# Kernel optimization log

Measured on AMD Instinct MI355X. Metric: run time of the kernel, lower is better.

The kernel has to match this reference:

```python
import jax, jax.numpy as jnp
import numpy as np

N = 20000
E = 320000
IN_DIM, HID, MID, OUT, HEADS = 1536, 512, 128, 5, 8
NEG_SLOPE = 0.2
BN_EPS = 1e-5


def gat_conv(x, edge_index, W, a_src, a_dst, bias, heads, out_ch):
    """PyG-style GATConv (eval mode, self-loops already in edge_index).
    x: [N, F_in]; W: [F_in, heads*out_ch]; a_src/a_dst: [heads, out_ch]; bias: [heads*out_ch].
    Returns [N, heads*out_ch] (head concat)."""
    n = x.shape[0]
    h = (x @ W).reshape(n, heads, out_ch)              # [N,H,C]
    src, dst = edge_index[0], edge_index[1]
    al_s = jnp.sum(h * a_src, axis=-1)                 # [N,H]
    al_d = jnp.sum(h * a_dst, axis=-1)                 # [N,H]
    e = al_s[src] + al_d[dst]                          # [E,H]
    e = jnp.where(e >= 0, e, NEG_SLOPE * e)            # leaky_relu
    # segment softmax over incoming edges per dst node
    e_max = jax.ops.segment_max(e, dst, num_segments=n)
    e_max = jnp.where(jnp.isfinite(e_max), e_max, 0.0)
    ex = jnp.exp(e - e_max[dst])                       # [E,H]
    denom = jax.ops.segment_sum(ex, dst, num_segments=n)
    alpha = ex / (denom[dst] + 1e-16)                  # [E,H]
    msg = h[src] * alpha[:, :, None]                   # [E,H,C]
    out = jax.ops.segment_sum(msg, dst, num_segments=n)
    return out.reshape(n, heads * out_ch) + bias


def bn_eval(x, gamma, beta, mean, var):
    return (x - mean) * jax.lax.rsqrt(var + BN_EPS) * gamma + beta


def setup_inputs() -> dict:
    key = jax.random.key(0)
    ks = jax.random.split(key, 24)
    x = jax.random.normal(ks[0], (N, IN_DIM), dtype=jnp.float32)
    edge_index = jax.random.randint(ks[1], (2, E), 0, N, dtype=jnp.int32)

    def glorot(k, shape):
        fan = shape[0] + shape[-1]
        return jax.random.normal(k, shape, dtype=jnp.float32) * np.sqrt(2.0 / fan)

    inp = {"x": x, "edge_index": edge_index}
    # conv1: 1536 -> 8 heads x 64
    inp["W1"] = glorot(ks[2], (IN_DIM, HID))
    inp["as1"] = glorot(ks[3], (HEADS, HID // HEADS))
    inp["ad1"] = glorot(ks[4], (HEADS, HID // HEADS))
    inp["b1"] = jnp.zeros((HID,), jnp.float32)
    # conv2: 512 -> 8 heads x 16
    inp["W2"] = glorot(ks[5], (HID, MID))
    inp["as2"] = glorot(ks[6], (HEADS, MID // HEADS))
    inp["ad2"] = glorot(ks[7], (HEADS, MID // HEADS))
    inp["b2"] = jnp.zeros((MID,), jnp.float32)
    # conv3: 128 -> 1 head x 5
    inp["W3"] = glorot(ks[8], (MID, OUT))
    inp["as3"] = glorot(ks[9], (1, OUT))
    inp["ad3"] = glorot(ks[10], (1, OUT))
    inp["b3"] = jnp.zeros((OUT,), jnp.float32)
    # batchnorm params (eval mode, running stats)
    inp["g1"] = jax.random.normal(ks[11], (HID,), jnp.float32) * 0.1 + 1.0
    inp["be1"] = jax.random.normal(ks[12], (HID,), jnp.float32) * 0.1
    inp["m1"] = jax.random.normal(ks[13], (HID,), jnp.float32) * 0.1
    inp["v1"] = jax.random.uniform(ks[14], (HID,), jnp.float32, 0.5, 1.5)
    inp["g2"] = jax.random.normal(ks[15], (MID,), jnp.float32) * 0.1 + 1.0
    inp["be2"] = jax.random.normal(ks[16], (MID,), jnp.float32) * 0.1
    inp["m2"] = jax.random.normal(ks[17], (MID,), jnp.float32) * 0.1
    inp["v2"] = jax.random.uniform(ks[18], (MID,), jnp.float32, 0.5, 1.5)
    return inp


def reference(x, edge_index, W1, as1, ad1, b1, W2, as2, ad2, b2, W3, as3, ad3, b3,
              g1, be1, m1, v1, g2, be2, m2, v2):
    # add self-loops (PyG GATConv default)
    loops = jnp.arange(N, dtype=edge_index.dtype)
    ei = jnp.concatenate([edge_index, jnp.stack([loops, loops])], axis=1)

    h = jax.nn.relu(gat_conv(x, ei, W1, as1, ad1, b1, HEADS, HID // HEADS))
    h = bn_eval(h, g1, be1, m1, v1)
    h = jax.nn.relu(gat_conv(h, ei, W2, as2, ad2, b2, HEADS, MID // HEADS))
    h = bn_eval(h, g2, be2, m2, v2)
    h = gat_conv(h, ei, W3, as3, ad3, b3, 1, OUT)
    return jax.nn.log_softmax(h, axis=1)
```

## Files before the change

### kernel.cpp

```cpp
#include <hip/hip_runtime.h>
#include <math.h>

#define IN_DIM 1536
#define HID 512
#define MID 128
#define OUTC 5
#define HEADS 8
#define NEG_SLOPE 0.2f
#define BN_EPS 1e-5f

typedef __attribute__((ext_vector_type(8))) short s16x8;
typedef __attribute__((ext_vector_type(4))) float fx4;

__device__ __forceinline__ unsigned short bf16_rne(float f) {
    unsigned int u = __float_as_uint(f);
    u += 0x7fffu + ((u >> 16) & 1u);
    return (unsigned short)(u >> 16);
}
__device__ __forceinline__ float bf16_to_f32(unsigned short u) {
    return __uint_as_float((unsigned int)u << 16);
}

__device__ __forceinline__ void async_copy16(void* lds, const void* g) {
    __builtin_amdgcn_global_load_lds(
        (const __attribute__((address_space(1))) unsigned int*)g,
        (__attribute__((address_space(3))) unsigned int*)lds, 16, 0, 0);
}

__global__ void hist_kernel(const int* __restrict__ ei, int* __restrict__ deg,
                            int ET, int E) {
    int e = blockIdx.x * blockDim.x + threadIdx.x;
    if (e >= ET) return;
    int dst = (e < E) ? ei[E + e] : (e - E);
    atomicAdd(&deg[dst], 1);
}

__global__ __launch_bounds__(1024) void scan_kernel(const int* __restrict__ deg,
                                                    int* __restrict__ row_ptr,
                                                    int* __restrict__ cursor, int n) {
    __shared__ int sdata[20000];
    __shared__ int partial[1024];
    int tid = threadIdx.x;
    for (int i = tid; i < n; i += 1024) sdata[i] = deg[i];
    __syncthreads();
    int per = (n + 1023) / 1024;
    int base = tid * per;
    int s = 0;
    for (int i = 0; i < per; ++i) {
        int idx = base + i;
        if (idx < n) s += sdata[idx];
    }
    partial[tid] = s;
    __syncthreads();
    for (int off = 1; off < 1024; off <<= 1) {
        int v = (tid >= off) ? partial[tid - off] : 0;
        __syncthreads();
        partial[tid] += v;
        __syncthreads();
    }
    int prefix = (tid == 0) ? 0 : partial[tid - 1];
    for (int i = 0; i < per; ++i) {
        int idx = base + i;
        if (idx < n) {
            int d = sdata[idx];
            sdata[idx] = prefix;
            prefix += d;
        }
    }
    __syncthreads();
    for (int i = tid; i < n; i += 1024) {
        int v = sdata[i];
        row_ptr[i] = v;
        cursor[i] = v;
    }
    if (tid == 1023) row_ptr[n] = partial[1023];
}

__global__ void scatter_kernel(const int* __restrict__ ei, int* __restrict__ cursor,
                               int* __restrict__ csr_src, int ET, int E) {
    int e = blockIdx.x * blockDim.x + threadIdx.x;
    if (e >= ET) return;
    int src, dst;
    if (e < E) { src = ei[e]; dst = ei[E + e]; }
    else       { src = dst = e - E; }
    int slot = atomicAdd(&cursor[dst], 1);
    csr_src[slot] = src;
}

#define ZB 20
__global__ __launch_bounds__(256) void prep_kernel(
    int* __restrict__ deg, int n_deg4,
    const float* __restrict__ W1, unsigned short* __restrict__ W1h,
    const float* __restrict__ W2, unsigned short* __restrict__ W2h,
    unsigned short* __restrict__ W2l,
    const float* __restrict__ x, unsigned short* __restrict__ xh, int n4) {
    int b = blockIdx.x;
    if (b < ZB) {
        int i = b * 256 + threadIdx.x;
        if (i < n_deg4) ((int4*)deg)[i] = make_int4(0, 0, 0, 0);
        return;
    }
    if (b < ZB + 832) {
        __shared__ float tile[32][33];
        int tb = b - ZB;
        const float* W;
        unsigned short *Th, *Tl;
        int K, Nn, kb, nb;
        bool wlo;
        if (tb < 768) {
            W = W1; Th = W1h; Tl = nullptr; wlo = false; K = IN_DIM; Nn = HID;
            nb = (tb & 15) * 32; kb = (tb >> 4) * 32;
        } else {
            int b2 = tb - 768;
            W = W2; Th = W2h; Tl = W2l; wlo = true; K = HID; Nn = MID;
            nb = (b2 & 3) * 32; kb = (b2 >> 2) * 32;
        }
        int tx = threadIdx.x & 31, ty = threadIdx.x >> 5;
#pragma unroll
        for (int r = 0; r < 4; ++r)
            tile[ty + r * 8][tx] = W[(size_t)(kb + ty + r * 8) * Nn + nb + tx];
        __syncthreads();
#pragma unroll
        for (int r = 0; r < 4; ++r) {
            int n = ty + r * 8;
            float v = tile[tx][n];
            unsigned short hi = bf16_rne(v);
            size_t o = (size_t)(nb + n) * K + kb + tx;
            Th[o] = hi;
            if (wlo) {
                float hif = __uint_as_float((unsigned int)hi << 16);
                Tl[o] = bf16_rne(v - hif);
            }
        }
        return;
    }
    int i = (b - ZB - 832) * 256 + threadIdx.x;
    if (i >= n4) return;
    float4 v = ((const float4*)x)[i];
    ushort4 o;
    o.x = bf16_rne(v.x); o.y = bf16_rne(v.y);
    o.z = bf16_rne(v.z); o.w = bf16_rne(v.w);
    ((ushort4*)xh)[i] = o;
}

__global__ __launch_bounds__(256) void gemm1_kernel(
    const unsigned short* __restrict__ A, const unsigned short* __restrict__ Bh,
    unsigned short* __restrict__ Cb, const float* __restrict__ a_s,
    const float* __restrict__ a_d, float* __restrict__ als,
    float* __restrict__ ald, int M, int N, int K, int MBLK) {
    int b = blockIdx.x;
    int xm = (b & 7) + 8 * (b >> 4);
    int ym = (b >> 3) & 1;
    if (xm >= MBLK) return;

    __shared__ unsigned short Asb[2][64 * 32];
    __shared__ unsigned short Bsb[2][256 * 32];

    const int tid = threadIdx.x;
    const int lane = tid & 63;
    const int wv = tid >> 6;
    const int row0 = xm * 64;
    const int nb0 = ym * 256;
    const int col = lane & 15;
    const int quad = lane >> 4;
    const int n0 = wv * 64;

    const int s_row = lane >> 2;
    const int s_chunk = (lane & 3) ^ ((lane >> 3) & 3);
    int agr = row0 + wv * 16 + s_row; if (agr >= M) agr = M - 1;
    const size_t ag = (size_t)agr * K + s_chunk * 8;
    size_t bg[4];
#pragma unroll
    for (int t = 0; t < 4; ++t)
        bg[t] = (size_t)(nb0 + (wv * 4 + t) * 16 + s_row) * K + s_chunk * 8;

    const int rsw = (col >> 1) & 3;

    fx4 acc[4][4];
#pragma unroll
    for (int i = 0; i < 4; ++i)
#pragma unroll
        for (int j = 0; j < 4; ++j) acc[i][j] = (fx4){0.f, 0.f, 0.f, 0.f};

    async_copy16(&Asb[0][wv * 512], A + ag);
#pragma unroll
    for (int t = 0; t < 4; ++t)
        async_copy16(&Bsb[0][(wv * 4 + t) * 512], Bh + bg[t]);
    __syncthreads();

    int cur = 0;
    for (int k0 = 0; k0 < K; k0 += 32) {
        const int nxt = cur ^ 1;
        if (k0 + 32 < K) {
            const int kn = k0 + 32;
            async_copy16(&Asb[nxt][wv * 512], A + ag + kn);
#pragma unroll
            for (int t = 0; t < 4; ++t)
                async_copy16(&Bsb[nxt][(wv * 4 + t) * 512], Bh + bg[t] + kn);
        }
        s16x8 afr[4], bfr[4];
#pragma unroll
        for (int i = 0; i < 4; ++i)
            afr[i] = *(const s16x8*)&Asb[cur][(i * 16 + col) * 32 + (quad ^ rsw) * 8];
#pragma unroll
        for (int j = 0; j < 4; ++j)
            bfr[j] = *(const s16x8*)&Bsb[cur][(n0 + j * 16 + col) * 32 + (quad ^ rsw) * 8];
#pragma unroll
        for (int i = 0; i < 4; ++i)
#pragma unroll
            for (int j = 0; j < 4; ++j)
                acc[i][j] = __builtin_amdgcn_mfma_f32_16x16x32_bf16(afr[i], bfr[j], acc[i][j], 0, 0, 0);
        __syncthreads();
        cur = nxt;
    }

#pragma unroll
    for (int i = 0; i < 4; ++i) {
        int gr0 = row0 + i * 16 + quad * 4;
#pragma unroll
        for (int j = 0; j < 4; ++j) {
            int gc = nb0 + n0 + j * 16 + col;
#pragma unroll
            for (int r = 0; r < 4; ++r) {
                int gr = gr0 + r;
                if (gr < M) Cb[(size_t)gr * N + gc] = bf16_rne(acc[i][j][r]);
            }
        }
    }

    const int head = (nb0 + n0) >> 6;
    float asv[4], adv[4];
#pragma unroll
    for (int j = 0; j < 4; ++j) {
        asv[j] = a_s[head * 64 + j * 16 + col];
        adv[j] = a_d[head * 64 + j * 16 + col];
    }
#pragma unroll
    for (int i = 0; i < 4; ++i) {
#pragma unroll
        for (int r = 0; r < 4; ++r) {
            float ss = acc[i][0][r] * asv[0] + acc[i][1][r] * asv[1] +
                       acc[i][2][r] * asv[2] + acc[i][3][r] * asv[3];
            float sd = acc[i][0][r] * adv[0] + acc[i][1][r] * adv[1] +
                       acc[i][2][r] * adv[2] + acc[i][3][r] * adv[3];
#pragma unroll
            for (int off = 8; off; off >>= 1) {
                ss += __shfl_xor(ss, off);
                sd += __shfl_xor(sd, off);
            }
            if (col == 0) {
                int gr = row0 + i * 16 + quad * 4 + r;
                if (gr < M) {
                    als[gr * HEADS + head] = ss;
                    ald[gr * HEADS + head] = sd;
                }
            }
        }
    }
}

__global__ __launch_bounds__(256) void gemm2_kernel(
    const unsigned short* __restrict__ A, const unsigned short* __restrict__ Bh,
    const unsigned short* __restrict__ Bl, unsigned short* __restrict__ Cb,
    const float* __restrict__ a_s, const float* __restrict__ a_d,
    float* __restrict__ als, float* __restrict__ ald, int M, int N, int K) {
    __shared__ unsigned short Asb[2][32 * 32];
    __shared__ unsigned short Bhb[2][128 * 32];
    __shared__ unsigned short Blb[2][128 * 32];

    const int tid = threadIdx.x;
    const int lane = tid & 63;
    const int wv = tid >> 6;
    const int row0 = blockIdx.x * 32;
    const int col = lane & 15;
    const int quad = lane >> 4;
    const int m0 = (wv >> 1) * 16;
    const int n0 = (wv & 1) * 64;
    const int b_row = lane >> 2;
    const int b_chunk = (lane & 3) ^ ((lane >> 3) & 3);
    const int rsw = (col >> 1) & 3;

    const int t0 = wv * 2, t1 = t0 + 1;
    const size_t bgo0 = (size_t)(t0 * 16 + b_row) * K + b_chunk * 8;
    const size_t bgo1 = (size_t)(t1 * 16 + b_row) * K + b_chunk * 8;
    int agr = row0 + wv * 16 + b_row; if (agr >= M) agr = M - 1;
    const size_t ago = (size_t)agr * K + b_chunk * 8;

    fx4 acc[4];
#pragma unroll
    for (int j = 0; j < 4; ++j) acc[j] = (fx4){0.f, 0.f, 0.f, 0.f};

    auto stage = [&](int buf, int k) {
        async_copy16(&Bhb[buf][t0 * 512], Bh + bgo0 + k);
        async_copy16(&Bhb[buf][t1 * 512], Bh + bgo1 + k);
        async_copy16(&Blb[buf][t0 * 512], Bl + bgo0 + k);
        async_copy16(&Blb[buf][t1 * 512], Bl + bgo1 + k);
        if (wv < 2) async_copy16(&Asb[buf][wv * 512], A + ago + k);
    };

    stage(0, 0);
    __syncthreads();

    int cur = 0;
    for (int k0 = 0; k0 < K; k0 += 32) {
        const int nxt = cur ^ 1;
        if (k0 + 32 < K) stage(nxt, k0 + 32);
        s16x8 a, bh4[4], bl4[4];
        a = *(const s16x8*)&Asb[cur][(m0 + col) * 32 + (quad ^ rsw) * 8];
#pragma unroll
        for (int j = 0; j < 4; ++j) {
            int rb = (n0 + j * 16 + col) * 32 + (quad ^ rsw) * 8;
            bh4[j] = *(const s16x8*)&Bhb[cur][rb];
            bl4[j] = *(const s16x8*)&Blb[cur][rb];
        }
#pragma unroll
        for (int j = 0; j < 4; ++j) {
            acc[j] = __builtin_amdgcn_mfma_f32_16x16x32_bf16(a, bl4[j], acc[j], 0, 0, 0);
            acc[j] = __builtin_amdgcn_mfma_f32_16x16x32_bf16(a, bh4[j], acc[j], 0, 0, 0);
        }
        __syncthreads();
        cur = nxt;
    }

    int gr0 = row0 + m0 + quad * 4;
#pragma unroll
    for (int j = 0; j < 4; ++j) {
        int gc = n0 + j * 16 + col;
#pragma unroll
        for (int r = 0; r < 4; ++r) {
            int gr = gr0 + r;
            if (gr < M) Cb[(size_t)gr * N + gc] = bf16_rne(acc[j][r]);
        }
    }

    float asv[4], adv[4];
#pragma unroll
    for (int j = 0; j < 4; ++j) {
        asv[j] = a_s[n0 + j * 16 + col];
        adv[j] = a_d[n0 + j * 16 + col];
    }
#pragma unroll
    for (int j = 0; j < 4; ++j) {
        int head = (n0 >> 4) + j;
#pragma unroll
        for (int r = 0; r < 4; ++r) {
            float ss = acc[j][r] * asv[j];
            float sd = acc[j][r] * adv[j];
#pragma unroll
            for (int off = 8; off; off >>= 1) {
                ss += __shfl_xor(ss, off);
                sd += __shfl_xor(sd, off);
            }
            if (col == 0) {
                int gr = gr0 + r;
                if (gr < M) {
                    als[gr * HEADS + head] = ss;
                    ald[gr * HEADS + head] = sd;
                }
            }
        }
    }
}

__global__ __launch_bounds__(256) void agg1_wave_kernel(
    const unsigned short* __restrict__ hlin, const float* __restrict__ als,
    const float* __restrict__ ald, const int* __restrict__ row_ptr,
    const int* __restrict__ csr_src, const float* __restrict__ bias,
    const float* __restrict__ gamma, const float* __restrict__ beta,
    const float* __restrict__ mean, const float* __restrict__ var,
    unsigned short* __restrict__ outh, int n) {
    int lane = threadIdx.x & 63;
    int dst = blockIdx.x * 4 + (threadIdx.x >> 6);
    if (dst >= n) return;
    const int f0 = lane * 8;
    const int h = lane >> 3;
    const int j8 = lane >> 3;
    const int ch = lane & 7;
    float ald_c = ald[dst * HEADS + ch];

    int s0 = row_ptr[dst], s1 = row_ptr[dst + 1];
    float acc[8];
#pragma unroll
    for (int v = 0; v < 8; ++v) acc[v] = 0.f;
    float den = 0.f;

    for (int base = s0; base < s1; base += 8) {
        int take = min(8, s1 - base);
        float ex = 0.f;
        int src_l = 0;
        if (j8 < take) {
            src_l = csr_src[base + j8];
            float e = als[src_l * HEADS + ch] + ald_c;
            e = (e >= 0.f) ? e : NEG_SLOPE * e;
            ex = __expf(e);
        }
        s16x8 rows[8];
#pragma unroll
        for (int jj = 0; jj < 8; ++jj) {
            if (jj < take) {
                int src = __shfl(src_l, jj * 8);
                rows[jj] = *(const s16x8*)&hlin[(size_t)src * HID + f0];
            }
        }
#pragma unroll
        for (int jj = 0; jj < 8; ++jj) {
            if (jj < take) {
                float a = __shfl(ex, jj * 8 + h);
                den += a;
                union { s16x8 v; unsigned short u[8]; } w;
                w.v = rows[jj];
#pragma unroll
                for (int v = 0; v < 8; ++v) acc[v] += a * bf16_to_f32(w.u[v]);
            }
        }
    }

    float rd = 1.f / (den + 1e-16f);
    union { s16x8 v; unsigned short u[8]; } o;
#pragma unroll
    for (int v = 0; v < 8; ++v) {
        int f = f0 + v;
        float val = acc[v] * rd + bias[f];
        val = fmaxf(val, 0.f);
        val = (val - mean[f]) * rsqrtf(var[f] + BN_EPS) * gamma[f] + beta[f];
        o.u[v] = bf16_rne(val);
    }
    *(s16x8*)&outh[(size_t)dst * HID + f0] = o.v;
}

__global__ __launch_bounds__(256) void agg2_l3_wave_kernel(
    const unsigned short* __restrict__ hlin, const float* __restrict__ als,
    const float* __restrict__ ald, const int* __restrict__ row_ptr,
    const int* __restrict__ csr_src, const float* __restrict__ bias,
    const float* __restrict__ gamma, const float* __restrict__ beta,
    const float* __restrict__ mean, const float* __restrict__ var,
    const float* __restrict__ W3, const float* __restrict__ as3,
    const float* __restrict__ ad3, float* __restrict__ h3lin,
    float* __restrict__ als3, float* __restrict__ ald3, int n) {
    int lane = threadIdx.x & 63;
    int dst = blockIdx.x * 4 + (threadIdx.x >> 6);
    if (dst >= n) return;
    const int f0 = lane * 2;
    const int h = lane >> 3;
    const int j8 = lane >> 3;
    const int ch = lane & 7;
    float ald_c = ald[dst * HEADS + ch];

    int s0 = row_ptr[dst], s1 = row_ptr[dst + 1];
    float acc0 = 0.f, acc1 = 0.f, den = 0.f;

    for (int base = s0; base < s1; base += 8) {
        int take = min(8, s1 - base);
        float ex = 0.f;
        int src_l = 0;
        if (j8 < take) {
            src_l = csr_src[base + j8];
            float e = als[src_l * HEADS + ch] + ald_c;
            e = (e >= 0.f) ? e : NEG_SLOPE * e;
            ex = __expf(e);
        }
        unsigned int rows[8];
#pragma unroll
        for (int jj = 0; jj < 8; ++jj) {
            if (jj < take) {
                int src = __shfl(src_l, jj * 8);
                rows[jj] = *(const unsigned int*)&hlin[(size_t)src * MID + f0];
            }
        }
#pragma unroll
        for (int jj = 0; jj < 8; ++jj) {
            if (jj < take) {
                float a = __shfl(ex, jj * 8 + h);
                den += a;
                acc0 += a * bf16_to_f32((unsigned short)(rows[jj] & 0xffffu));
                acc1 += a * bf16_to_f32((unsigned short)(rows[jj] >> 16));
            }
        }
    }

    float rd = 1.f / (den + 1e-16f);
    float val0 = acc0 * rd + bias[f0];
    val0 = fmaxf(val0, 0.f);
    val0 = (val0 - mean[f0]) * rsqrtf(var[f0] + BN_EPS) * gamma[f0] + beta[f0];
    float val1 = acc1 * rd + bias[f0 + 1];
    val1 = fmaxf(val1, 0.f);
    val1 = (val1 - mean[f0 + 1]) * rsqrtf(var[f0 + 1] + BN_EPS) * gamma[f0 + 1] + beta[f0 + 1];

    float p[OUTC];
#pragma unroll
    for (int c = 0; c < OUTC; ++c)
        p[c] = val0 * W3[f0 * OUTC + c] + val1 * W3[(f0 + 1) * OUTC + c];
#pragma unroll
    for (int off = 32; off; off >>= 1) {
#pragma unroll
        for (int c = 0; c < OUTC; ++c) p[c] += __shfl_xor(p[c], off);
    }
    if (lane == 0) {
        float ss = 0.f, sd = 0.f;
#pragma unroll
        for (int c = 0; c < OUTC; ++c) {
            h3lin[(size_t)dst * OUTC + c] = p[c];
            ss += p[c] * as3[c];
            sd += p[c] * ad3[c];
        }
        als3[dst] = ss;
        ald3[dst] = sd;
    }
}

__global__ __launch_bounds__(256) void agg3_lsm_kernel(
    const float* __restrict__ h3lin, const float* __restrict__ als,
    const float* __restrict__ ald, const int* __restrict__ row_ptr,
    const int* __restrict__ csr_src, const float* __restrict__ b3,
    float* __restrict__ out, int n) {
    int g = blockIdx.x * blockDim.x + threadIdx.x;
    int dst = g >> 4;
    int l = g & 15;
    if (dst >= n) return;
    int s0 = row_ptr[dst], s1 = row_ptr[dst + 1];
    float ad = ald[dst];
    float den = 0.f;
    float acc[OUTC] = {0.f, 0.f, 0.f, 0.f, 0.f};
    for (int j = s0 + l; j < s1; j += 16) {
        int src = csr_src[j];
        float e = als[src] + ad;
        e = (e >= 0.f) ? e : NEG_SLOPE * e;
        float x = __expf(e);
        den += x;
        const float* hp = h3lin + (size_t)src * OUTC;
#pragma unroll
        for (int c = 0; c < OUTC; ++c) acc[c] += x * hp[c];
    }
#pragma unroll
    for (int off = 8; off; off >>= 1) {
        den += __shfl_xor(den, off);
#pragma unroll
        for (int c = 0; c < OUTC; ++c) acc[c] += __shfl_xor(acc[c], off);
    }
    if (l == 0) {
        float rd = 1.f / (den + 1e-16f);
        float m = -INFINITY;
#pragma unroll
        for (int c = 0; c < OUTC; ++c) {
            acc[c] = acc[c] * rd + b3[c];
            m = fmaxf(m, acc[c]);
        }
        float s = 0.f;
#pragma unroll
        for (int c = 0; c < OUTC; ++c) s += __expf(acc[c] - m);
        float lse = m + __logf(s);
#pragma unroll
        for (int c = 0; c < OUTC; ++c) out[(size_t)dst * OUTC + c] = acc[c] - lse;
    }
}

extern "C" void kernel_launch(void* const* d_in, const int* in_sizes, int n_in,
                              void* d_out, int out_size, void* d_ws, size_t ws_size,
                              hipStream_t stream) {
    const float* x   = (const float*)d_in[0];
    const int*   ei  = (const int*)d_in[1];
    const float* W1  = (const float*)d_in[2];
    const float* as1 = (const float*)d_in[3];
    const float* ad1 = (const float*)d_in[4];
    const float* b1  = (const float*)d_in[5];
    const float* W2  = (const float*)d_in[6];
    const float* as2 = (const float*)d_in[7];
    const float* ad2 = (const float*)d_in[8];
    const float* b2  = (const float*)d_in[9];
    const float* W3  = (const float*)d_in[10];
    const float* as3 = (const float*)d_in[11];
    const float* ad3 = (const float*)d_in[12];
    const float* b3  = (const float*)d_in[13];
    const float* g1  = (const float*)d_in[14];
    const float* be1 = (const float*)d_in[15];
    const float* m1  = (const float*)d_in[16];
    const float* v1  = (const float*)d_in[17];
    const float* g2  = (const float*)d_in[18];
    const float* be2 = (const float*)d_in[19];
    const float* m2  = (const float*)d_in[20];
    const float* v2  = (const float*)d_in[21];

    const int N = in_sizes[0] / IN_DIM;
    const int E = in_sizes[1] / 2;
    const int ET = E + N;
    const int MBLK1 = (N + 63) / 64;
    const int MBLK2 = (N + 31) / 32;

    char* ws = (char*)d_ws;
    size_t off = 0;
    auto take = [&](size_t bytes) -> char* {
        char* p = ws + off;
        off += (bytes + 255) & ~(size_t)255;
        return p;
    };
    int* deg      = (int*)take((size_t)N * 4);
    int* row_ptr  = (int*)take((size_t)(N + 1) * 4);
    int* cursor   = (int*)take((size_t)N * 4);
    int* csr_src  = (int*)take((size_t)ET * 4);
    unsigned short* W1h = (unsigned short*)take((size_t)HID * IN_DIM * 2);
    unsigned short* W2h = (unsigned short*)take((size_t)MID * HID * 2);
    unsigned short* W2l = (unsigned short*)take((size_t)MID * HID * 2);
    unsigned short* xh  = (unsigned short*)take((size_t)N * IN_DIM * 2);
    unsigned short* h1lin = (unsigned short*)take((size_t)N * HID * 2);
    unsigned short* h1h   = (unsigned short*)take((size_t)N * HID * 2);
    unsigned short* h2lin = (unsigned short*)take((size_t)N * MID * 2);
    float* h3lin  = (float*)take((size_t)N * OUTC * 4);
    float* als    = (float*)take((size_t)N * HEADS * 4);
    float* ald    = (float*)take((size_t)N * HEADS * 4);
    float* als3   = (float*)take((size_t)N * 4);
    float* ald3   = (float*)take((size_t)N * 4);

    {
        int n4 = N * IN_DIM / 4;
        int nb_cvt = (n4 + 255) / 256;
        prep_kernel<<<ZB + 832 + nb_cvt, 256, 0, stream>>>(
            deg, N / 4, W1, W1h, W2, W2h, W2l, x, xh, n4);
    }
    hist_kernel<<<(ET + 255) / 256, 256, 0, stream>>>(ei, deg, ET, E);
    scan_kernel<<<1, 1024, 0, stream>>>(deg, row_ptr, cursor, N);
    scatter_kernel<<<(ET + 255) / 256, 256, 0, stream>>>(ei, cursor, csr_src, ET, E);

    gemm1_kernel<<<640, 256, 0, stream>>>(xh, W1h, h1lin, as1, ad1, als, ald,
                                          N, HID, IN_DIM, MBLK1);
    agg1_wave_kernel<<<(N + 3) / 4, 256, 0, stream>>>(
        h1lin, als, ald, row_ptr, csr_src, b1, g1, be1, m1, v1, h1h, N);

    gemm2_kernel<<<MBLK2, 256, 0, stream>>>(h1h, W2h, W2l, h2lin, as2, ad2,
                                            als, ald, N, MID, HID);
    agg2_l3_wave_kernel<<<(N + 3) / 4, 256, 0, stream>>>(
        h2lin, als, ald, row_ptr, csr_src, b2, g2, be2, m2, v2,
        W3, as3, ad3, h3lin, als3, ald3, N);

    agg3_lsm_kernel<<<(N * 16 + 255) / 256, 256, 0, stream>>>(
        h3lin, als3, ald3, row_ptr, csr_src, b3, (float*)d_out, N);
}
```

Measured before the change: 431.1 us.

## Widen GEMM tiles: full-N block for gemm1, 128-row tiles for gemm2

```diff
diff --git a/kernel.cpp b/kernel.cpp
--- a/kernel.cpp
+++ b/kernel.cpp
@@ -143,36 +143,30 @@
     ((ushort4*)xh)[i] = o;
 }
 
-__global__ __launch_bounds__(256) void gemm1_kernel(
+__global__ __launch_bounds__(512) void gemm1_kernel(
     const unsigned short* __restrict__ A, const unsigned short* __restrict__ Bh,
     unsigned short* __restrict__ Cb, const float* __restrict__ a_s,
     const float* __restrict__ a_d, float* __restrict__ als,
-    float* __restrict__ ald, int M, int N, int K, int MBLK) {
-    int b = blockIdx.x;
-    int xm = (b & 7) + 8 * (b >> 4);
-    int ym = (b >> 3) & 1;
-    if (xm >= MBLK) return;
-
+    float* __restrict__ ald, int M, int N, int K) {
     __shared__ unsigned short Asb[2][64 * 32];
-    __shared__ unsigned short Bsb[2][256 * 32];
+    __shared__ unsigned short Bsb[2][512 * 32];
 
     const int tid = threadIdx.x;
     const int lane = tid & 63;
     const int wv = tid >> 6;
-    const int row0 = xm * 64;
-    const int nb0 = ym * 256;
+    const int row0 = blockIdx.x * 64;
     const int col = lane & 15;
     const int quad = lane >> 4;
     const int n0 = wv * 64;
 
     const int s_row = lane >> 2;
     const int s_chunk = (lane & 3) ^ ((lane >> 3) & 3);
-    int agr = row0 + wv * 16 + s_row; if (agr >= M) agr = M - 1;
+    int agr = row0 + (wv & 3) * 16 + s_row; if (agr >= M) agr = M - 1;
     const size_t ag = (size_t)agr * K + s_chunk * 8;
     size_t bg[4];
 #pragma unroll
     for (int t = 0; t < 4; ++t)
-        bg[t] = (size_t)(nb0 + (wv * 4 + t) * 16 + s_row) * K + s_chunk * 8;
+        bg[t] = (size_t)(wv * 64 + t * 16 + s_row) * K + s_chunk * 8;
 
     const int rsw = (col >> 1) & 3;
 
@@ -182,7 +176,7 @@
 #pragma unroll
         for (int j = 0; j < 4; ++j) acc[i][j] = (fx4){0.f, 0.f, 0.f, 0.f};
 
-    async_copy16(&Asb[0][wv * 512], A + ag);
+    if (wv < 4) async_copy16(&Asb[0][wv * 512], A + ag);
 #pragma unroll
     for (int t = 0; t < 4; ++t)
         async_copy16(&Bsb[0][(wv * 4 + t) * 512], Bh + bg[t]);
@@ -193,7 +187,7 @@
         const int nxt = cur ^ 1;
         if (k0 + 32 < K) {
             const int kn = k0 + 32;
-            async_copy16(&Asb[nxt][wv * 512], A + ag + kn);
+            if (wv < 4) async_copy16(&Asb[nxt][wv * 512], A + ag + kn);
 #pragma unroll
             for (int t = 0; t < 4; ++t)
                 async_copy16(&Bsb[nxt][(wv * 4 + t) * 512], Bh + bg[t] + kn);
@@ -219,7 +213,7 @@
         int gr0 = row0 + i * 16 + quad * 4;
 #pragma unroll
         for (int j = 0; j < 4; ++j) {
-            int gc = nb0 + n0 + j * 16 + col;
+            int gc = n0 + j * 16 + col;
 #pragma unroll
             for (int r = 0; r < 4; ++r) {
                 int gr = gr0 + r;
@@ -228,7 +222,7 @@
         }
     }
 
-    const int head = (nb0 + n0) >> 6;
+    const int head = wv;
     float asv[4], adv[4];
 #pragma unroll
     for (int j = 0; j < 4; ++j) {
@@ -264,38 +258,43 @@
     const unsigned short* __restrict__ Bl, unsigned short* __restrict__ Cb,
     const float* __restrict__ a_s, const float* __restrict__ a_d,
     float* __restrict__ als, float* __restrict__ ald, int M, int N, int K) {
-    __shared__ unsigned short Asb[2][32 * 32];
+    __shared__ unsigned short Asb[2][128 * 32];
     __shared__ unsigned short Bhb[2][128 * 32];
     __shared__ unsigned short Blb[2][128 * 32];
 
     const int tid = threadIdx.x;
     const int lane = tid & 63;
     const int wv = tid >> 6;
-    const int row0 = blockIdx.x * 32;
+    const int row0 = blockIdx.x * 128;
     const int col = lane & 15;
     const int quad = lane >> 4;
-    const int m0 = (wv >> 1) * 16;
+    const int m0 = (wv >> 1) * 64;
     const int n0 = (wv & 1) * 64;
-    const int b_row = lane >> 2;
-    const int b_chunk = (lane & 3) ^ ((lane >> 3) & 3);
+    const int s_row = lane >> 2;
+    const int s_chunk = (lane & 3) ^ ((lane >> 3) & 3);
     const int rsw = (col >> 1) & 3;
 
     const int t0 = wv * 2, t1 = t0 + 1;
-    const size_t bgo0 = (size_t)(t0 * 16 + b_row) * K + b_chunk * 8;
-    const size_t bgo1 = (size_t)(t1 * 16 + b_row) * K + b_chunk * 8;
-    int agr = row0 + wv * 16 + b_row; if (agr >= M) agr = M - 1;
-    const size_t ago = (size_t)agr * K + b_chunk * 8;
-
-    fx4 acc[4];
-#pragma unroll
-    for (int j = 0; j < 4; ++j) acc[j] = (fx4){0.f, 0.f, 0.f, 0.f};
+    int agr0 = row0 + t0 * 16 + s_row; if (agr0 >= M) agr0 = M - 1;
+    int agr1 = row0 + t1 * 16 + s_row; if (agr1 >= M) agr1 = M - 1;
+    const size_t ag0 = (size_t)agr0 * K + s_chunk * 8;
+    const size_t ag1 = (size_t)agr1 * K + s_chunk * 8;
+    const size_t bg0 = (size_t)(t0 * 16 + s_row) * K + s_chunk * 8;
+    const size_t bg1 = (size_t)(t1 * 16 + s_row) * K + s_chunk * 8;
+
+    fx4 acc[4][4];
+#pragma unroll
+    for (int i = 0; i < 4; ++i)
+#pragma unroll
+        for (int j = 0; j < 4; ++j) acc[i][j] = (fx4){0.f, 0.f, 0.f, 0.f};
 
     auto stage = [&](int buf, int k) {
-        async_copy16(&Bhb[buf][t0 * 512], Bh + bgo0 + k);
-        async_copy16(&Bhb[buf][t1 * 512], Bh + bgo1 + k);
-        async_copy16(&Blb[buf][t0 * 512], Bl + bgo0 + k);
-        async_copy16(&Blb[buf][t1 * 512], Bl + bgo1 + k);
-        if (wv < 2) async_copy16(&Asb[buf][wv * 512], A + ago + k);
+        async_copy16(&Asb[buf][t0 * 512], A + ag0 + k);
+        async_copy16(&Asb[buf][t1 * 512], A + ag1 + k);
+        async_copy16(&Bhb[buf][t0 * 512], Bh + bg0 + k);
+        async_copy16(&Bhb[buf][t1 * 512], Bh + bg1 + k);
+        async_copy16(&Blb[buf][t0 * 512], Bl + bg0 + k);
+        async_copy16(&Blb[buf][t1 * 512], Bl + bg1 + k);
     };
 
     stage(0, 0);
@@ -305,8 +304,10 @@
     for (int k0 = 0; k0 < K; k0 += 32) {
         const int nxt = cur ^ 1;
         if (k0 + 32 < K) stage(nxt, k0 + 32);
-        s16x8 a, bh4[4], bl4[4];
-        a = *(const s16x8*)&Asb[cur][(m0 + col) * 32 + (quad ^ rsw) * 8];
+        s16x8 afr[4], bh4[4], bl4[4];
+#pragma unroll
+        for (int i = 0; i < 4; ++i)
+            afr[i] = *(const s16x8*)&Asb[cur][(m0 + i * 16 + col) * 32 + (quad ^ rsw) * 8];
 #pragma unroll
         for (int j = 0; j < 4; ++j) {
             int rb = (n0 + j * 16 + col) * 32 + (quad ^ rsw) * 8;
@@ -314,22 +315,27 @@
             bl4[j] = *(const s16x8*)&Blb[cur][rb];
         }
 #pragma unroll
-        for (int j = 0; j < 4; ++j) {
-            acc[j] = __builtin_amdgcn_mfma_f32_16x16x32_bf16(a, bl4[j], acc[j], 0, 0, 0);
-            acc[j] = __builtin_amdgcn_mfma_f32_16x16x32_bf16(a, bh4[j], acc[j], 0, 0, 0);
-        }
+        for (int i = 0; i < 4; ++i)
+#pragma unroll
+            for (int j = 0; j < 4; ++j) {
+                acc[i][j] = __builtin_amdgcn_mfma_f32_16x16x32_bf16(afr[i], bl4[j], acc[i][j], 0, 0, 0);
+                acc[i][j] = __builtin_amdgcn_mfma_f32_16x16x32_bf16(afr[i], bh4[j], acc[i][j], 0, 0, 0);
+            }
         __syncthreads();
         cur = nxt;
     }
 
-    int gr0 = row0 + m0 + quad * 4;
-#pragma unroll
-    for (int j = 0; j < 4; ++j) {
-        int gc = n0 + j * 16 + col;
-#pragma unroll
-        for (int r = 0; r < 4; ++r) {
-            int gr = gr0 + r;
-            if (gr < M) Cb[(size_t)gr * N + gc] = bf16_rne(acc[j][r]);
+#pragma unroll
+    for (int i = 0; i < 4; ++i) {
+        int gr0 = row0 + m0 + i * 16 + quad * 4;
+#pragma unroll
+        for (int j = 0; j < 4; ++j) {
+            int gc = n0 + j * 16 + col;
+#pragma unroll
+            for (int r = 0; r < 4; ++r) {
+                int gr = gr0 + r;
+                if (gr < M) Cb[(size_t)gr * N + gc] = bf16_rne(acc[i][j][r]);
+            }
         }
     }
 
@@ -340,22 +346,26 @@
         adv[j] = a_d[n0 + j * 16 + col];
     }
 #pragma unroll
-    for (int j = 0; j < 4; ++j) {
-        int head = (n0 >> 4) + j;
-#pragma unroll
-        for (int r = 0; r < 4; ++r) {
-            float ss = acc[j][r] * asv[j];
-            float sd = acc[j][r] * adv[j];
-#pragma unroll
-            for (int off = 8; off; off >>= 1) {
-                ss += __shfl_xor(ss, off);
-                sd += __shfl_xor(sd, off);
-            }
-            if (col == 0) {
-                int gr = gr0 + r;
-                if (gr < M) {
-                    als[gr * HEADS + head] = ss;
-                    ald[gr * HEADS + head] = sd;
+    for (int i = 0; i < 4; ++i) {
+        int gr0 = row0 + m0 + i * 16 + quad * 4;
+#pragma unroll
+        for (int j = 0; j < 4; ++j) {
+            int head = (n0 >> 4) + j;
+#pragma unroll
+            for (int r = 0; r < 4; ++r) {
+                float ss = acc[i][j][r] * asv[j];
+                float sd = acc[i][j][r] * adv[j];
+#pragma unroll
+                for (int off = 8; off; off >>= 1) {
+                    ss += __shfl_xor(ss, off);
+                    sd += __shfl_xor(sd, off);
+                }
+                if (col == 0) {
+                    int gr = gr0 + r;
+                    if (gr < M) {
+                        als[gr * HEADS + head] = ss;
+                        ald[gr * HEADS + head] = sd;
+                    }
                 }
             }
         }
@@ -584,7 +594,7 @@
     const int E = in_sizes[1] / 2;
     const int ET = E + N;
     const int MBLK1 = (N + 63) / 64;
-    const int MBLK2 = (N + 31) / 32;
+    const int MBLK2 = (N + 127) / 128;
 
     char* ws = (char*)d_ws;
     size_t off = 0;
@@ -620,8 +630,8 @@
     scan_kernel<<<1, 1024, 0, stream>>>(deg, row_ptr, cursor, N);
     scatter_kernel<<<(ET + 255) / 256, 256, 0, stream>>>(ei, cursor, csr_src, ET, E);
 
-    gemm1_kernel<<<640, 256, 0, stream>>>(xh, W1h, h1lin, as1, ad1, als, ald,
-                                          N, HID, IN_DIM, MBLK1);
+    gemm1_kernel<<<MBLK1, 512, 0, stream>>>(xh, W1h, h1lin, as1, ad1, als, ald,
+                                            N, HID, IN_DIM);
     agg1_wave_kernel<<<(N + 3) / 4, 256, 0, stream>>>(
         h1lin, als, ald, row_ptr, csr_src, b1, g1, be1, m1, v1, h1h, N);
 
```

Result: slower. 447.4 us (+3.8%).

## Fuse degree histogram into prep kernel and CSR scatter into GEMM1 launch

Applied to the files above, without the earlier changes.

```diff
diff --git a/kernel.cpp b/kernel.cpp
--- a/kernel.cpp
+++ b/kernel.cpp
@@ -25,14 +25,6 @@
     __builtin_amdgcn_global_load_lds(
         (const __attribute__((address_space(1))) unsigned int*)g,
         (__attribute__((address_space(3))) unsigned int*)lds, 16, 0, 0);
-}
-
-__global__ void hist_kernel(const int* __restrict__ ei, int* __restrict__ deg,
-                            int ET, int E) {
-    int e = blockIdx.x * blockDim.x + threadIdx.x;
-    if (e >= ET) return;
-    int dst = (e < E) ? ei[E + e] : (e - E);
-    atomicAdd(&deg[dst], 1);
 }
 
 __global__ __launch_bounds__(1024) void scan_kernel(const int* __restrict__ deg,
@@ -76,33 +68,24 @@
     if (tid == 1023) row_ptr[n] = partial[1023];
 }
 
-__global__ void scatter_kernel(const int* __restrict__ ei, int* __restrict__ cursor,
-                               int* __restrict__ csr_src, int ET, int E) {
-    int e = blockIdx.x * blockDim.x + threadIdx.x;
-    if (e >= ET) return;
-    int src, dst;
-    if (e < E) { src = ei[e]; dst = ei[E + e]; }
-    else       { src = dst = e - E; }
-    int slot = atomicAdd(&cursor[dst], 1);
-    csr_src[slot] = src;
-}
-
-#define ZB 20
 __global__ __launch_bounds__(256) void prep_kernel(
-    int* __restrict__ deg, int n_deg4,
+    const int* __restrict__ ei, int* __restrict__ deg, int ET, int E, int HB,
     const float* __restrict__ W1, unsigned short* __restrict__ W1h,
     const float* __restrict__ W2, unsigned short* __restrict__ W2h,
     unsigned short* __restrict__ W2l,
     const float* __restrict__ x, unsigned short* __restrict__ xh, int n4) {
     int b = blockIdx.x;
-    if (b < ZB) {
-        int i = b * 256 + threadIdx.x;
-        if (i < n_deg4) ((int4*)deg)[i] = make_int4(0, 0, 0, 0);
+    if (b < HB) {
+        int e = b * 256 + threadIdx.x;
+        if (e < ET) {
+            int dst = (e < E) ? ei[E + e] : (e - E);
+            atomicAdd(&deg[dst], 1);
+        }
         return;
     }
-    if (b < ZB + 832) {
+    if (b < HB + 832) {
         __shared__ float tile[32][33];
-        int tb = b - ZB;
+        int tb = b - HB;
         const float* W;
         unsigned short *Th, *Tl;
         int K, Nn, kb, nb;
@@ -134,7 +117,7 @@
         }
         return;
     }
-    int i = (b - ZB - 832) * 256 + threadIdx.x;
+    int i = (b - HB - 832) * 256 + threadIdx.x;
     if (i >= n4) return;
     float4 v = ((const float4*)x)[i];
     ushort4 o;
@@ -143,12 +126,25 @@
     ((ushort4*)xh)[i] = o;
 }
 
-__global__ __launch_bounds__(256) void gemm1_kernel(
+__global__ __launch_bounds__(256) void gemm1_scatter_kernel(
     const unsigned short* __restrict__ A, const unsigned short* __restrict__ Bh,
     unsigned short* __restrict__ Cb, const float* __restrict__ a_s,
     const float* __restrict__ a_d, float* __restrict__ als,
-    float* __restrict__ ald, int M, int N, int K, int MBLK) {
+    float* __restrict__ ald, int M, int N, int K, int MBLK,
+    const int* __restrict__ ei, int* __restrict__ cursor,
+    int* __restrict__ csr_src, int ET, int E, int GB) {
     int b = blockIdx.x;
+    if (b >= GB) {
+        int e = (b - GB) * 256 + threadIdx.x;
+        if (e < ET) {
+            int src, dst;
+            if (e < E) { src = ei[e]; dst = ei[E + e]; }
+            else       { src = dst = e - E; }
+            int slot = atomicAdd(&cursor[dst], 1);
+            csr_src[slot] = src;
+        }
+        return;
+    }
     int xm = (b & 7) + 8 * (b >> 4);
     int ym = (b >> 3) & 1;
     if (xm >= MBLK) return;
@@ -585,6 +581,7 @@
     const int ET = E + N;
     const int MBLK1 = (N + 63) / 64;
     const int MBLK2 = (N + 31) / 32;
+    const int HB = (ET + 255) / 256;
 
     char* ws = (char*)d_ws;
     size_t off = 0;
@@ -610,18 +607,18 @@
     float* als3   = (float*)take((size_t)N * 4);
     float* ald3   = (float*)take((size_t)N * 4);
 
+    hipMemsetAsync(deg, 0, (size_t)N * 4, stream);
     {
         int n4 = N * IN_DIM / 4;
         int nb_cvt = (n4 + 255) / 256;
-        prep_kernel<<<ZB + 832 + nb_cvt, 256, 0, stream>>>(
-            deg, N / 4, W1, W1h, W2, W2h, W2l, x, xh, n4);
-    }
-    hist_kernel<<<(ET + 255) / 256, 256, 0, stream>>>(ei, deg, ET, E);
+        prep_kernel<<<HB + 832 + nb_cvt, 256, 0, stream>>>(
+            ei, deg, ET, E, HB, W1, W1h, W2, W2h, W2l, x, xh, n4);
+    }
     scan_kernel<<<1, 1024, 0, stream>>>(deg, row_ptr, cursor, N);
-    scatter_kernel<<<(ET + 255) / 256, 256, 0, stream>>>(ei, cursor, csr_src, ET, E);
-
-    gemm1_kernel<<<640, 256, 0, stream>>>(xh, W1h, h1lin, as1, ad1, als, ald,
-                                          N, HID, IN_DIM, MBLK1);
+
+    gemm1_scatter_kernel<<<640 + HB, 256, 0, stream>>>(
+        xh, W1h, h1lin, as1, ad1, als, ald, N, HID, IN_DIM, MBLK1,
+        ei, cursor, csr_src, ET, E, 640);
     agg1_wave_kernel<<<(N + 3) / 4, 256, 0, stream>>>(
         h1lin, als, ald, row_ptr, csr_src, b1, g1, be1, m1, v1, h1h, N);
 
```

Measured after the change: 411.2 us. 1.05x faster.
